# Kernel optimization log

Hardware: AMD Instinct MI355X
Metric: run time of the kernel (lower is better)

Reference implementation:

```python
import jax, jax.numpy as jnp
import numpy as np

N_NODES = 100000
N_EDGES = 1600000
D_IN = 128
D_OUT = 128


def setup_inputs() -> dict:
    key = jax.random.key(0)
    k1, k2, k3, k4 = jax.random.split(key, 4)
    feat = jax.random.normal(k1, (N_NODES, D_IN), dtype=jnp.float32)
    # xavier_uniform on [D_IN, D_OUT]
    limit = float(np.sqrt(6.0 / (D_IN + D_OUT)))
    weight = jax.random.uniform(k2, (D_IN, D_OUT), minval=-limit, maxval=limit, dtype=jnp.float32)
    bias = jnp.zeros((D_OUT,), dtype=jnp.float32)
    src = jax.random.randint(k3, (N_EDGES,), 0, N_NODES, dtype=jnp.int32)
    dst = jax.random.randint(k4, (N_EDGES,), 0, N_NODES, dtype=jnp.int32)
    return {"feat": feat, "weight": weight, "bias": bias, "src": src, "dst": dst}


def reference(feat, weight, bias, src, dst):
    n = feat.shape[0]
    # in-degree of each node (number of incoming edges)
    deg = jax.ops.segment_sum(jnp.ones_like(dst, dtype=feat.dtype), dst, num_segments=n)
    norm = jnp.power(jnp.clip(deg, 1.0), -0.5)[:, None]  # [N, 1]
    # pre-normalize source features
    h = feat * norm
    # copy_src + sum aggregation: scatter-add messages from src to dst
    agg = jax.ops.segment_sum(h[src], dst, num_segments=n)  # [N, D_IN]
    # in_feats == out_feats -> matmul after aggregation (the else-branch)
    rst = jnp.matmul(agg, weight)
    rst = rst * norm + bias
    return rst
```

## Files before the change

### kernel.cpp

```cpp
#include <hip/hip_runtime.h>

#define D 128
#define BSHIFT 7
#define BNODES 128
#define BMASK 127
#define NB_MAX 1024
#define STRIDE 2944
#define BIN_CHUNK 4096
#define GP_ROWS 64
#define GLDP 132

typedef unsigned int uint;
typedef __attribute__((ext_vector_type(8))) short bf16x8;
typedef __attribute__((ext_vector_type(4))) float f32x4;

__device__ inline uint bf16_rne(float x) {
    uint u = __float_as_uint(x);
    return (u + 0x7fffu + ((u >> 16) & 1u)) >> 16;
}
__device__ inline uint pack2(float lo, float hi) {
    return bf16_rne(lo) | (bf16_rne(hi) << 16);
}

__global__ void __launch_bounds__(256) init_kernel(int* __restrict__ bucket_cur,
                                                   const float* __restrict__ W,
                                                   uint4* __restrict__ wpack) {
    int t = threadIdx.x;
    if (blockIdx.x == 0) {
        for (int j = t; j < NB_MAX; j += 256) bucket_cur[j] = 0;
    } else {
        for (int idx = t; idx < 2048; idx += 256) {
            int lane = idx & 63;
            int ks = (idx >> 6) & 3;
            int ct = idx >> 8;
            int col = ct * 16 + (lane & 15);
            int k0 = ks * 32 + (lane >> 4) * 8;
            uint4 u;
            u.x = pack2(W[(k0 + 0) * D + col], W[(k0 + 1) * D + col]);
            u.y = pack2(W[(k0 + 2) * D + col], W[(k0 + 3) * D + col]);
            u.z = pack2(W[(k0 + 4) * D + col], W[(k0 + 5) * D + col]);
            u.w = pack2(W[(k0 + 6) * D + col], W[(k0 + 7) * D + col]);
            wpack[idx] = u;
        }
    }
}

__global__ void __launch_bounds__(256) mega_kernel(
        const int* __restrict__ src, const int* __restrict__ dst,
        int* __restrict__ bucket_cur, uint* __restrict__ binned,
        const float* __restrict__ feat, const uint4* __restrict__ wpack,
        uint* __restrict__ g32, int n_edges, int nchunks, int n) {
    __shared__ float As[GP_ROWS][GLDP];
    int t = threadIdx.x;

    if (blockIdx.x < (uint)nchunks) {
        int* h = (int*)&As[0][0];
        int* base = h + NB_MAX;
        long long e0 = (long long)blockIdx.x * BIN_CHUNK;
        for (int j = t; j < NB_MAX; j += 256) h[j] = 0;
        __syncthreads();

        int d[16], s[16];
#pragma unroll
        for (int k = 0; k < 16; ++k) {
            long long idx = e0 + k * 256 + t;
            if (idx < n_edges) {
                d[k] = dst[idx];
                s[k] = src[idx];
                atomicAdd(&h[d[k] >> BSHIFT], 1);
            } else {
                d[k] = -1;
            }
        }
        __syncthreads();
        for (int j = t; j < NB_MAX; j += 256) {
            int c = h[j];
            base[j] = c ? atomicAdd(&bucket_cur[j], c) : 0;
            h[j] = 0;
        }
        __syncthreads();
#pragma unroll
        for (int k = 0; k < 16; ++k) {
            if (d[k] >= 0) {
                int b = d[k] >> BSHIFT;
                int r = base[b] + atomicAdd(&h[b], 1);
                if (r < STRIDE)
                    binned[(size_t)b * STRIDE + r] =
                        ((uint)s[k] << BSHIFT) | (uint)(d[k] & BMASK);
            }
        }
        return;
    }

    int lane = t & 63;
    int w = t >> 6;
    int r0 = (blockIdx.x - nchunks) * GP_ROWS;

    for (int idx = t; idx < GP_ROWS * 32; idx += 256) {
        int row = idx >> 5;
        int p = idx & 31;
        int gr = r0 + row;
        if (gr >= n) gr = n - 1;
        float4 f = *(const float4*)(feat + (size_t)gr * D + p * 4);
        *(float4*)&As[row][p * 4] = f;
    }
    __syncthreads();

    int c = lane & 15;
    int g = lane >> 4;
    int rbase = w * 16;

    uint4 afr[4];
#pragma unroll
    for (int ks = 0; ks < 4; ++ks) {
        const float* ap = &As[rbase + c][ks * 32 + g * 8];
        float4 f0 = *(const float4*)ap;
        float4 f1 = *(const float4*)(ap + 4);
        afr[ks].x = pack2(f0.x, f0.y);
        afr[ks].y = pack2(f0.z, f0.w);
        afr[ks].z = pack2(f1.x, f1.y);
        afr[ks].w = pack2(f1.z, f1.w);
    }

#pragma unroll
    for (int ct = 0; ct < 8; ++ct) {
        f32x4 acc = {0.f, 0.f, 0.f, 0.f};
#pragma unroll
        for (int ks = 0; ks < 4; ++ks) {
            uint4 bu = wpack[(ct * 4 + ks) * 64 + lane];
            acc = __builtin_amdgcn_mfma_f32_16x16x32_bf16(
                *(bf16x8*)&afr[ks], *(bf16x8*)&bu, acc, 0, 0, 0);
        }
#pragma unroll
        for (int r = 0; r < 4; ++r)
            As[rbase + g * 4 + r][ct * 16 + c] = acc[r];
    }

    for (int idx = lane; idx < 16 * 64; idx += 64) {
        int row = idx >> 6;
        int j = idx & 63;
        int gr = r0 + rbase + row;
        if (gr < n) {
            uint vpk = pack2(As[rbase + row][2 * j], As[rbase + row][2 * j + 1]);
            g32[(size_t)gr * 64 + j] = vpk;
        }
    }
}

__global__ void __launch_bounds__(256) fill2_kernel(
        const int* __restrict__ bucket_cur, uint* __restrict__ csr,
        int* __restrict__ row_start, int* __restrict__ degp,
        float* __restrict__ norm, int n_nodes) {
    __shared__ uint sbin[STRIDE];
    __shared__ int deg[BNODES];
    __shared__ int rs[BNODES];
    __shared__ int cur[BNODES];
    int b = blockIdx.x;
    int t = threadIdx.x;
    int cnt = bucket_cur[b];
    if (cnt > STRIDE) cnt = STRIDE;
    size_t gbase = (size_t)b * STRIDE;

    for (int k = t; k < cnt; k += 256) sbin[k] = csr[gbase + k];
    if (t < BNODES) deg[t] = 0;
    __syncthreads();
    for (int k = t; k < cnt; k += 256) atomicAdd(&deg[sbin[k] & BMASK], 1);
    __syncthreads();

    int v = 0;
    if (t < BNODES) {
        v = deg[t];
        rs[t] = v;
    }
    __syncthreads();
    for (int o = 1; o < BNODES; o <<= 1) {
        int a = (t < BNODES && t >= o) ? rs[t - o] : 0;
        __syncthreads();
        if (t < BNODES) rs[t] += a;
        __syncthreads();
    }
    if (t < BNODES) {
        int excl = rs[t] - v;
        rs[t] = excl;
        cur[t] = 0;
        int node = b * BNODES + t;
        if (node < n_nodes) {
            row_start[node] = (int)gbase + excl;
            degp[node] = v;
            norm[node] = rsqrtf(fmaxf((float)v, 1.0f));
        }
    }
    __syncthreads();

    for (int k = t; k < cnt; k += 256) {
        uint p = sbin[k];
        int dl = p & BMASK;
        int r = atomicAdd(&cur[dl], 1);
        csr[gbase + rs[dl] + r] = p >> BSHIFT;
    }
}

#define UNPACK_FMA(u, nmv)                                   \
    acc[0] += __uint_as_float((u).x << 16) * (nmv);          \
    acc[1] += __uint_as_float((u).x & 0xffff0000u) * (nmv);  \
    acc[2] += __uint_as_float((u).y << 16) * (nmv);          \
    acc[3] += __uint_as_float((u).y & 0xffff0000u) * (nmv);  \
    acc[4] += __uint_as_float((u).z << 16) * (nmv);          \
    acc[5] += __uint_as_float((u).z & 0xffff0000u) * (nmv);  \
    acc[6] += __uint_as_float((u).w << 16) * (nmv);          \
    acc[7] += __uint_as_float((u).w & 0xffff0000u) * (nmv);

__global__ void __launch_bounds__(256) gather_out_kernel(
        const uint4* __restrict__ g128, const uint* __restrict__ csr,
        const int* __restrict__ row_start, const int* __restrict__ degp,
        const float* __restrict__ norm, const float* __restrict__ bias,
        float* __restrict__ out, int n) {
    int lane = threadIdx.x & 63;
    int wid = threadIdx.x >> 6;
    int i = blockIdx.x * 4 + wid;
    if (i >= n) return;
    int g = lane >> 4;
    int c = lane & 15;
    float4 b_lo = *(const float4*)(bias + 8 * c);
    float4 b_hi = *(const float4*)(bias + 8 * c + 4);

    int beg = row_start[i];
    int dv = degp[i];
    int end = beg + dv;
    float acc[8];
#pragma unroll
    for (int j = 0; j < 8; ++j) acc[j] = 0.f;

    for (int base = beg; base < end; base += 64) {
        int nk = end - base;
        if (nk > 64) nk = 64;
        int epre = (base + lane < end) ? (int)csr[base + lane] : 0;
        float npre = norm[epre];
        int k = 0;
        int kfull = nk & ~7;
        for (; k < kfull; k += 8) {
            int s0 = __shfl(epre, k + g, 64);
            int s1 = __shfl(epre, k + 4 + g, 64);
            float nm0 = __shfl(npre, k + g, 64);
            float nm1 = __shfl(npre, k + 4 + g, 64);
            uint4 u0 = g128[(size_t)s0 * 16 + c];
            uint4 u1 = g128[(size_t)s1 * 16 + c];
            UNPACK_FMA(u0, nm0);
            UNPACK_FMA(u1, nm1);
        }
        if (k < nk) {
            int e0 = k + g;
            int e1 = k + 4 + g;
            int s0 = __shfl(epre, e0 & 63, 64);
            int s1 = __shfl(epre, e1 & 63, 64);
            float nm0 = __shfl(npre, e0 & 63, 64);
            float nm1 = __shfl(npre, e1 & 63, 64);
            uint4 z = {0u, 0u, 0u, 0u};
            uint4 u0 = (e0 < nk) ? g128[(size_t)s0 * 16 + c] : z;
            uint4 u1 = (e1 < nk) ? g128[(size_t)s1 * 16 + c] : z;
            UNPACK_FMA(u0, nm0);
            UNPACK_FMA(u1, nm1);
        }
    }

#pragma unroll
    for (int j = 0; j < 8; ++j) {
        acc[j] += __shfl_xor(acc[j], 16, 64);
        acc[j] += __shfl_xor(acc[j], 32, 64);
    }
    if (g == 0) {
        float nrm = rsqrtf(fmaxf((float)dv, 1.0f));
        float4 lo, hi;
        lo.x = acc[0] * nrm + b_lo.x;
        lo.y = acc[1] * nrm + b_lo.y;
        lo.z = acc[2] * nrm + b_lo.z;
        lo.w = acc[3] * nrm + b_lo.w;
        hi.x = acc[4] * nrm + b_hi.x;
        hi.y = acc[5] * nrm + b_hi.y;
        hi.z = acc[6] * nrm + b_hi.z;
        hi.w = acc[7] * nrm + b_hi.w;
        float* orow = out + (size_t)i * D + 8 * c;
        *(float4*)orow = lo;
        *(float4*)(orow + 4) = hi;
    }
}

extern "C" void kernel_launch(void* const* d_in, const int* in_sizes, int n_in,
                              void* d_out, int out_size, void* d_ws, size_t ws_size,
                              hipStream_t stream) {
    const float* feat   = (const float*)d_in[0];
    const float* weight = (const float*)d_in[1];
    const float* bias   = (const float*)d_in[2];
    const int*   src    = (const int*)d_in[3];
    const int*   dst    = (const int*)d_in[4];
    float* out = (float*)d_out;

    int n_nodes = in_sizes[0] / D;
    int n_edges = in_sizes[3];
    int nb = (n_nodes + BNODES - 1) >> BSHIFT;
    int nchunks = (n_edges + BIN_CHUNK - 1) / BIN_CHUNK;
    int ngemm = (n_nodes + GP_ROWS - 1) / GP_ROWS;

    float* norm       = (float*)d_ws;
    int*   degp       = (int*)(norm + n_nodes);
    int*   row_start  = degp + n_nodes;
    int*   bucket_cur = row_start + n_nodes;
    uint*  csr        = (uint*)(bucket_cur + NB_MAX);
    uint*  g32        = csr + (size_t)nb * STRIDE;
    uint4* wpack      = (uint4*)(g32 + (size_t)n_nodes * 64);

    init_kernel<<<2, 256, 0, stream>>>(bucket_cur, weight, wpack);
    mega_kernel<<<nchunks + ngemm, 256, 0, stream>>>(
        src, dst, bucket_cur, csr, feat, wpack, g32, n_edges, nchunks, n_nodes);
    fill2_kernel<<<nb, 256, 0, stream>>>(bucket_cur, csr, row_start, degp, norm,
                                         n_nodes);
    gather_out_kernel<<<(n_nodes + 3) / 4, 256, 0, stream>>>(
        (const uint4*)g32, csr, row_start, degp, norm, bias, out, n_nodes);
}
```

Before: 120.4 us.

## Split GEMM tiles across binning and CSR-fill kernels to overlap work

New measurement: 124.0 us. 1.03x slower.

```diff
diff --git a/kernel.cpp b/kernel.cpp
--- a/kernel.cpp
+++ b/kernel.cpp
@@ -45,7 +45,66 @@
     }
 }
 
-__global__ void __launch_bounds__(256) mega_kernel(
+__device__ __forceinline__ void gemm_tile(float (*As)[GLDP],
+                                          const float* __restrict__ feat,
+                                          const uint4* __restrict__ wpack,
+                                          uint* __restrict__ g32, int r0, int n,
+                                          int t) {
+    int lane = t & 63;
+    int w = t >> 6;
+
+    for (int idx = t; idx < GP_ROWS * 32; idx += 256) {
+        int row = idx >> 5;
+        int p = idx & 31;
+        int gr = r0 + row;
+        if (gr >= n) gr = n - 1;
+        float4 f = *(const float4*)(feat + (size_t)gr * D + p * 4);
+        *(float4*)&As[row][p * 4] = f;
+    }
+    __syncthreads();
+
+    int c = lane & 15;
+    int g = lane >> 4;
+    int rbase = w * 16;
+
+    uint4 afr[4];
+#pragma unroll
+    for (int ks = 0; ks < 4; ++ks) {
+        const float* ap = &As[rbase + c][ks * 32 + g * 8];
+        float4 f0 = *(const float4*)ap;
+        float4 f1 = *(const float4*)(ap + 4);
+        afr[ks].x = pack2(f0.x, f0.y);
+        afr[ks].y = pack2(f0.z, f0.w);
+        afr[ks].z = pack2(f1.x, f1.y);
+        afr[ks].w = pack2(f1.z, f1.w);
+    }
+
+#pragma unroll
+    for (int ct = 0; ct < 8; ++ct) {
+        f32x4 acc = {0.f, 0.f, 0.f, 0.f};
+#pragma unroll
+        for (int ks = 0; ks < 4; ++ks) {
+            uint4 bu = wpack[(ct * 4 + ks) * 64 + lane];
+            acc = __builtin_amdgcn_mfma_f32_16x16x32_bf16(
+                *(bf16x8*)&afr[ks], *(bf16x8*)&bu, acc, 0, 0, 0);
+        }
+#pragma unroll
+        for (int r = 0; r < 4; ++r)
+            As[rbase + g * 4 + r][ct * 16 + c] = acc[r];
+    }
+
+    for (int idx = lane; idx < 16 * 64; idx += 64) {
+        int row = idx >> 6;
+        int j = idx & 63;
+        int gr = r0 + rbase + row;
+        if (gr < n) {
+            uint vpk = pack2(As[rbase + row][2 * j], As[rbase + row][2 * j + 1]);
+            g32[(size_t)gr * 64 + j] = vpk;
+        }
+    }
+}
+
+__global__ void __launch_bounds__(256) megaA_kernel(
         const int* __restrict__ src, const int* __restrict__ dst,
         int* __restrict__ bucket_cur, uint* __restrict__ binned,
         const float* __restrict__ feat, const uint4* __restrict__ wpack,
@@ -92,112 +151,70 @@
         return;
     }
 
-    int lane = t & 63;
-    int w = t >> 6;
-    int r0 = (blockIdx.x - nchunks) * GP_ROWS;
-
-    for (int idx = t; idx < GP_ROWS * 32; idx += 256) {
-        int row = idx >> 5;
-        int p = idx & 31;
-        int gr = r0 + row;
-        if (gr >= n) gr = n - 1;
-        float4 f = *(const float4*)(feat + (size_t)gr * D + p * 4);
-        *(float4*)&As[row][p * 4] = f;
-    }
-    __syncthreads();
-
-    int c = lane & 15;
-    int g = lane >> 4;
-    int rbase = w * 16;
-
-    uint4 afr[4];
-#pragma unroll
-    for (int ks = 0; ks < 4; ++ks) {
-        const float* ap = &As[rbase + c][ks * 32 + g * 8];
-        float4 f0 = *(const float4*)ap;
-        float4 f1 = *(const float4*)(ap + 4);
-        afr[ks].x = pack2(f0.x, f0.y);
-        afr[ks].y = pack2(f0.z, f0.w);
-        afr[ks].z = pack2(f1.x, f1.y);
-        afr[ks].w = pack2(f1.z, f1.w);
-    }
-
-#pragma unroll
-    for (int ct = 0; ct < 8; ++ct) {
-        f32x4 acc = {0.f, 0.f, 0.f, 0.f};
-#pragma unroll
-        for (int ks = 0; ks < 4; ++ks) {
-            uint4 bu = wpack[(ct * 4 + ks) * 64 + lane];
-            acc = __builtin_amdgcn_mfma_f32_16x16x32_bf16(
-                *(bf16x8*)&afr[ks], *(bf16x8*)&bu, acc, 0, 0, 0);
-        }
-#pragma unroll
-        for (int r = 0; r < 4; ++r)
-            As[rbase + g * 4 + r][ct * 16 + c] = acc[r];
-    }
-
-    for (int idx = lane; idx < 16 * 64; idx += 64) {
-        int row = idx >> 6;
-        int j = idx & 63;
-        int gr = r0 + rbase + row;
-        if (gr < n) {
-            uint vpk = pack2(As[rbase + row][2 * j], As[rbase + row][2 * j + 1]);
-            g32[(size_t)gr * 64 + j] = vpk;
-        }
-    }
-}
-
-__global__ void __launch_bounds__(256) fill2_kernel(
+    gemm_tile(As, feat, wpack, g32, (int)(blockIdx.x - nchunks) * GP_ROWS, n, t);
+}
+
+__global__ void __launch_bounds__(256) megaB_kernel(
         const int* __restrict__ bucket_cur, uint* __restrict__ csr,
         int* __restrict__ row_start, int* __restrict__ degp,
-        float* __restrict__ norm, int n_nodes) {
-    __shared__ uint sbin[STRIDE];
-    __shared__ int deg[BNODES];
-    __shared__ int rs[BNODES];
-    __shared__ int cur[BNODES];
-    int b = blockIdx.x;
+        float* __restrict__ norm, const float* __restrict__ feat,
+        const uint4* __restrict__ wpack, uint* __restrict__ g32, int nb,
+        int ng_a, int n_nodes) {
+    __shared__ float As[GP_ROWS][GLDP];
     int t = threadIdx.x;
-    int cnt = bucket_cur[b];
-    if (cnt > STRIDE) cnt = STRIDE;
-    size_t gbase = (size_t)b * STRIDE;
-
-    for (int k = t; k < cnt; k += 256) sbin[k] = csr[gbase + k];
-    if (t < BNODES) deg[t] = 0;
-    __syncthreads();
-    for (int k = t; k < cnt; k += 256) atomicAdd(&deg[sbin[k] & BMASK], 1);
-    __syncthreads();
-
-    int v = 0;
-    if (t < BNODES) {
-        v = deg[t];
-        rs[t] = v;
-    }
-    __syncthreads();
-    for (int o = 1; o < BNODES; o <<= 1) {
-        int a = (t < BNODES && t >= o) ? rs[t - o] : 0;
-        __syncthreads();
-        if (t < BNODES) rs[t] += a;
-        __syncthreads();
-    }
-    if (t < BNODES) {
-        int excl = rs[t] - v;
-        rs[t] = excl;
-        cur[t] = 0;
-        int node = b * BNODES + t;
-        if (node < n_nodes) {
-            row_start[node] = (int)gbase + excl;
-            degp[node] = v;
-            norm[node] = rsqrtf(fmaxf((float)v, 1.0f));
-        }
-    }
-    __syncthreads();
-
-    for (int k = t; k < cnt; k += 256) {
-        uint p = sbin[k];
-        int dl = p & BMASK;
-        int r = atomicAdd(&cur[dl], 1);
-        csr[gbase + rs[dl] + r] = p >> BSHIFT;
-    }
+
+    if (blockIdx.x < (uint)nb) {
+        uint* sbin = (uint*)&As[0][0];
+        int* deg = (int*)(sbin + STRIDE);
+        int* rs = deg + BNODES;
+        int* cur = rs + BNODES;
+        int b = blockIdx.x;
+        int cnt = bucket_cur[b];
+        if (cnt > STRIDE) cnt = STRIDE;
+        size_t gbase = (size_t)b * STRIDE;
+
+        for (int k = t; k < cnt; k += 256) sbin[k] = csr[gbase + k];
+        if (t < BNODES) deg[t] = 0;
+        __syncthreads();
+        for (int k = t; k < cnt; k += 256) atomicAdd(&deg[sbin[k] & BMASK], 1);
+        __syncthreads();
+
+        int v = 0;
+        if (t < BNODES) {
+            v = deg[t];
+            rs[t] = v;
+        }
+        __syncthreads();
+        for (int o = 1; o < BNODES; o <<= 1) {
+            int a = (t < BNODES && t >= o) ? rs[t - o] : 0;
+            __syncthreads();
+            if (t < BNODES) rs[t] += a;
+            __syncthreads();
+        }
+        if (t < BNODES) {
+            int excl = rs[t] - v;
+            rs[t] = excl;
+            cur[t] = 0;
+            int node = b * BNODES + t;
+            if (node < n_nodes) {
+                row_start[node] = (int)gbase + excl;
+                degp[node] = v;
+                norm[node] = rsqrtf(fmaxf((float)v, 1.0f));
+            }
+        }
+        __syncthreads();
+
+        for (int k = t; k < cnt; k += 256) {
+            uint p = sbin[k];
+            int dl = p & BMASK;
+            int r = atomicAdd(&cur[dl], 1);
+            csr[gbase + rs[dl] + r] = p >> BSHIFT;
+        }
+        return;
+    }
+
+    gemm_tile(As, feat, wpack, g32,
+              (ng_a + (int)(blockIdx.x - nb)) * GP_ROWS, n_nodes, t);
 }
 
 #define UNPACK_FMA(u, nmv)                                   \
@@ -300,6 +317,8 @@
     int nb = (n_nodes + BNODES - 1) >> BSHIFT;
     int nchunks = (n_edges + BIN_CHUNK - 1) / BIN_CHUNK;
     int ngemm = (n_nodes + GP_ROWS - 1) / GP_ROWS;
+    int ng_a = ngemm / 2;
+    int ng_b = ngemm - ng_a;
 
     float* norm       = (float*)d_ws;
     int*   degp       = (int*)(norm + n_nodes);
@@ -310,10 +329,11 @@
     uint4* wpack      = (uint4*)(g32 + (size_t)n_nodes * 64);
 
     init_kernel<<<2, 256, 0, stream>>>(bucket_cur, weight, wpack);
-    mega_kernel<<<nchunks + ngemm, 256, 0, stream>>>(
+    megaA_kernel<<<nchunks + ng_a, 256, 0, stream>>>(
         src, dst, bucket_cur, csr, feat, wpack, g32, n_edges, nchunks, n_nodes);
-    fill2_kernel<<<nb, 256, 0, stream>>>(bucket_cur, csr, row_start, degp, norm,
-                                         n_nodes);
+    megaB_kernel<<<nb + ng_b, 256, 0, stream>>>(
+        bucket_cur, csr, row_start, degp, norm, feat, wpack, g32, nb, ng_a,
+        n_nodes);
     gather_out_kernel<<<(n_nodes + 3) / 4, 256, 0, stream>>>(
         (const uint4*)g32, csr, row_start, degp, norm, bias, out, n_nodes);
 }
```

## Split projected features into column-group slices and gather per slice

Applied to the files above, without the earlier changes.

After: 332.0 us. 176% more time.

```diff
diff --git a/kernel.cpp b/kernel.cpp
--- a/kernel.cpp
+++ b/kernel.cpp
@@ -95,6 +95,7 @@
     int lane = t & 63;
     int w = t >> 6;
     int r0 = (blockIdx.x - nchunks) * GP_ROWS;
+    size_t P = (size_t)n * 8;
 
     for (int idx = t; idx < GP_ROWS * 32; idx += 256) {
         int row = idx >> 5;
@@ -136,13 +137,15 @@
             As[rbase + g * 4 + r][ct * 16 + c] = acc[r];
     }
 
+    int cg = lane >> 3;
+    int wch = lane & 7;
     for (int idx = lane; idx < 16 * 64; idx += 64) {
         int row = idx >> 6;
-        int j = idx & 63;
         int gr = r0 + rbase + row;
         if (gr < n) {
-            uint vpk = pack2(As[rbase + row][2 * j], As[rbase + row][2 * j + 1]);
-            g32[(size_t)gr * 64 + j] = vpk;
+            uint vpk = pack2(As[rbase + row][2 * lane],
+                             As[rbase + row][2 * lane + 1]);
+            g32[(size_t)cg * P + (size_t)gr * 8 + wch] = vpk;
         }
     }
 }
@@ -200,88 +203,76 @@
     }
 }
 
-#define UNPACK_FMA(u, nmv)                                   \
-    acc[0] += __uint_as_float((u).x << 16) * (nmv);          \
-    acc[1] += __uint_as_float((u).x & 0xffff0000u) * (nmv);  \
-    acc[2] += __uint_as_float((u).y << 16) * (nmv);          \
-    acc[3] += __uint_as_float((u).y & 0xffff0000u) * (nmv);  \
-    acc[4] += __uint_as_float((u).z << 16) * (nmv);          \
-    acc[5] += __uint_as_float((u).z & 0xffff0000u) * (nmv);  \
-    acc[6] += __uint_as_float((u).w << 16) * (nmv);          \
-    acc[7] += __uint_as_float((u).w & 0xffff0000u) * (nmv);
-
 __global__ void __launch_bounds__(256) gather_out_kernel(
-        const uint4* __restrict__ g128, const uint* __restrict__ csr,
+        const uint* __restrict__ g32, const uint* __restrict__ csr,
         const int* __restrict__ row_start, const int* __restrict__ degp,
         const float* __restrict__ norm, const float* __restrict__ bias,
         float* __restrict__ out, int n) {
     int lane = threadIdx.x & 63;
     int wid = threadIdx.x >> 6;
-    int i = blockIdx.x * 4 + wid;
+    int cg = blockIdx.x & 7;
+    int i = (blockIdx.x >> 3) * 4 + wid;
     if (i >= n) return;
-    int g = lane >> 4;
-    int c = lane & 15;
-    float4 b_lo = *(const float4*)(bias + 8 * c);
-    float4 b_hi = *(const float4*)(bias + 8 * c + 4);
+    int g2 = lane >> 3;
+    int c2 = lane & 7;
+    size_t P = (size_t)n * 8;
+    const uint* slice = g32 + (size_t)cg * P;
 
     int beg = row_start[i];
     int dv = degp[i];
     int end = beg + dv;
-    float acc[8];
-#pragma unroll
-    for (int j = 0; j < 8; ++j) acc[j] = 0.f;
+    float a0 = 0.f, a1 = 0.f;
 
     for (int base = beg; base < end; base += 64) {
         int nk = end - base;
         if (nk > 64) nk = 64;
-        int epre = (base + lane < end) ? (int)csr[base + lane] : 0;
+        int epre = (base + lane < end)
+                       ? (int)__builtin_nontemporal_load(csr + base + lane)
+                       : 0;
         float npre = norm[epre];
         int k = 0;
-        int kfull = nk & ~7;
-        for (; k < kfull; k += 8) {
-            int s0 = __shfl(epre, k + g, 64);
-            int s1 = __shfl(epre, k + 4 + g, 64);
-            float nm0 = __shfl(npre, k + g, 64);
-            float nm1 = __shfl(npre, k + 4 + g, 64);
-            uint4 u0 = g128[(size_t)s0 * 16 + c];
-            uint4 u1 = g128[(size_t)s1 * 16 + c];
-            UNPACK_FMA(u0, nm0);
-            UNPACK_FMA(u1, nm1);
+        int kfull = nk & ~15;
+        for (; k < kfull; k += 16) {
+            int s0 = __shfl(epre, k + g2, 64);
+            float nm0 = __shfl(npre, k + g2, 64);
+            int s1 = __shfl(epre, k + 8 + g2, 64);
+            float nm1 = __shfl(npre, k + 8 + g2, 64);
+            uint u0 = slice[(size_t)s0 * 8 + c2];
+            uint u1 = slice[(size_t)s1 * 8 + c2];
+            a0 += __uint_as_float(u0 << 16) * nm0;
+            a1 += __uint_as_float(u0 & 0xffff0000u) * nm0;
+            a0 += __uint_as_float(u1 << 16) * nm1;
+            a1 += __uint_as_float(u1 & 0xffff0000u) * nm1;
         }
         if (k < nk) {
-            int e0 = k + g;
-            int e1 = k + 4 + g;
+            int e0 = k + g2;
+            int e1 = k + 8 + g2;
             int s0 = __shfl(epre, e0 & 63, 64);
+            float nm0 = __shfl(npre, e0 & 63, 64);
             int s1 = __shfl(epre, e1 & 63, 64);
-            float nm0 = __shfl(npre, e0 & 63, 64);
             float nm1 = __shfl(npre, e1 & 63, 64);
-            uint4 z = {0u, 0u, 0u, 0u};
-            uint4 u0 = (e0 < nk) ? g128[(size_t)s0 * 16 + c] : z;
-            uint4 u1 = (e1 < nk) ? g128[(size_t)s1 * 16 + c] : z;
-            UNPACK_FMA(u0, nm0);
-            UNPACK_FMA(u1, nm1);
-        }
-    }
-
-#pragma unroll
-    for (int j = 0; j < 8; ++j) {
-        acc[j] += __shfl_xor(acc[j], 16, 64);
-        acc[j] += __shfl_xor(acc[j], 32, 64);
-    }
-    if (g == 0) {
+            uint u0 = (e0 < nk) ? slice[(size_t)s0 * 8 + c2] : 0u;
+            uint u1 = (e1 < nk) ? slice[(size_t)s1 * 8 + c2] : 0u;
+            a0 += __uint_as_float(u0 << 16) * nm0;
+            a1 += __uint_as_float(u0 & 0xffff0000u) * nm0;
+            a0 += __uint_as_float(u1 << 16) * nm1;
+            a1 += __uint_as_float(u1 & 0xffff0000u) * nm1;
+        }
+    }
+
+    a0 += __shfl_xor(a0, 8, 64);
+    a0 += __shfl_xor(a0, 16, 64);
+    a0 += __shfl_xor(a0, 32, 64);
+    a1 += __shfl_xor(a1, 8, 64);
+    a1 += __shfl_xor(a1, 16, 64);
+    a1 += __shfl_xor(a1, 32, 64);
+
+    if (g2 == 0) {
         float nrm = rsqrtf(fmaxf((float)dv, 1.0f));
-        float4 lo, hi;
-        lo.x = acc[0] * nrm + b_lo.x;
-        lo.y = acc[1] * nrm + b_lo.y;
-        lo.z = acc[2] * nrm + b_lo.z;
-        lo.w = acc[3] * nrm + b_lo.w;
-        hi.x = acc[4] * nrm + b_hi.x;
-        hi.y = acc[5] * nrm + b_hi.y;
-        hi.z = acc[6] * nrm + b_hi.z;
-        hi.w = acc[7] * nrm + b_hi.w;
-        float* orow = out + (size_t)i * D + 8 * c;
-        *(float4*)orow = lo;
-        *(float4*)(orow + 4) = hi;
+        const float2 bv = *(const float2*)(bias + cg * 16 + 2 * c2);
+        float* p = out + (size_t)i * D + cg * 16 + 2 * c2;
+        __builtin_nontemporal_store(a0 * nrm + bv.x, p);
+        __builtin_nontemporal_store(a1 * nrm + bv.y, p + 1);
     }
 }
 
@@ -314,6 +305,6 @@
         src, dst, bucket_cur, csr, feat, wpack, g32, n_edges, nchunks, n_nodes);
     fill2_kernel<<<nb, 256, 0, stream>>>(bucket_cur, csr, row_start, degp, norm,
                                          n_nodes);
-    gather_out_kernel<<<(n_nodes + 3) / 4, 256, 0, stream>>>(
-        (const uint4*)g32, csr, row_start, degp, norm, bias, out, n_nodes);
-}
+    gather_out_kernel<<<((n_nodes + 3) / 4) * 8, 256, 0, stream>>>(
+        g32, csr, row_start, degp, norm, bias, out, n_nodes);
+}
```
